# Kernel optimization log

Hardware: AMD Instinct MI355X
Metric: run time of the kernel (lower is better)

The kernel has to match this reference:

```python
import jax, jax.numpy as jnp
import numpy as np

DIM = 1024
HEADS = 16
DIM_HEAD = 64
INNER = HEADS * DIM_HEAD
SCALE = 8.0  # default scale in plain_cosine_sim_attention
EPS = 1e-5


def setup_inputs() -> dict:
    key = jax.random.key(0)
    ks = jax.random.split(key, 5)
    b, n = 2, 2048
    x = jax.random.normal(ks[0], (b, n, DIM), dtype=jnp.float32)
    ln_w = jnp.ones((DIM,), dtype=jnp.float32)
    ln_b = jnp.zeros((DIM,), dtype=jnp.float32)
    W_qkv = jax.random.normal(ks[1], (DIM, 3 * INNER), dtype=jnp.float32) * (DIM ** -0.5)
    W_out = jax.random.normal(ks[2], (INNER, DIM), dtype=jnp.float32) * (INNER ** -0.5)
    return {"x": x, "ln_w": ln_w, "ln_b": ln_b, "W_qkv": W_qkv, "W_out": W_out}


def _l2norm(t):
    return t / jnp.clip(jnp.linalg.norm(t, axis=-1, keepdims=True), 1e-12)


def reference(x, ln_w, ln_b, W_qkv, W_out):
    b, n, _ = x.shape
    # LayerNorm
    mu = jnp.mean(x, axis=-1, keepdims=True)
    var = jnp.var(x, axis=-1, keepdims=True)
    xn = (x - mu) * jax.lax.rsqrt(var + EPS) * ln_w + ln_b
    # QKV projection (no bias)
    qkv = xn @ W_qkv  # [b, n, 3*inner]
    q, k, v = jnp.split(qkv, 3, axis=-1)
    # [b, n, h*d] -> [b, h, n, d]
    def to_heads(t):
        return t.reshape(b, n, HEADS, DIM_HEAD).transpose(0, 2, 1, 3)
    q, k, v = to_heads(q), to_heads(k), to_heads(v)
    # cosine-sim attention: l2-normalize q, k then scaled dot product
    q = _l2norm(q)
    k = _l2norm(k)
    sim = jnp.einsum('bhid,bhjd->bhij', q, k) * SCALE
    # causal mask
    causal = jnp.tril(jnp.ones((n, n), dtype=bool))
    sim = jnp.where(causal, sim, jnp.finfo(sim.dtype).min)
    attn = jax.nn.softmax(sim, axis=-1)
    o = jnp.einsum('bhij,bhjd->bhid', attn, v)
    # [b, h, n, d] -> [b, n, h*d]
    o = o.transpose(0, 2, 1, 3).reshape(b, n, INNER)
    return o @ W_out
```

## Files before the change

### kernel.cpp

```cpp
#include <hip/hip_runtime.h>
#include <hip/hip_bf16.h>

typedef __attribute__((ext_vector_type(8))) short short8;
typedef __attribute__((ext_vector_type(4))) float floatx4;

__device__ __forceinline__ ushort f2bf(float f) {
    union { __hip_bfloat16 h; ushort u; } cv;
    cv.h = __float2bfloat16(f);
    return cv.u;
}
__device__ __forceinline__ float bf2f(ushort u) {
    union { ushort u; __hip_bfloat16 h; } cv;
    cv.u = u;
    return __bfloat162float(cv.h);
}
__device__ __forceinline__ ushort f2bf_rtz(float f) {
    union { float f; unsigned u; } cv;
    cv.f = f;
    return (ushort)(cv.u >> 16);
}

typedef __attribute__((address_space(1))) void* gas1_t;
typedef __attribute__((address_space(3))) void* las3_t;
__device__ __forceinline__ void cp16(const ushort* g, ushort* l) {
    __builtin_amdgcn_global_load_lds((gas1_t)(unsigned long long)g,
                                     (las3_t)(unsigned long long)l, 16, 0, 0);
}

__global__ __launch_bounds__(256) void prep_w_ln(const float* __restrict__ Wqkv,
                                                 const float* __restrict__ Wout,
                                                 ushort* __restrict__ WqkvT,
                                                 ushort* __restrict__ WoutT,
                                                 const float* __restrict__ x,
                                                 const float* __restrict__ lw,
                                                 const float* __restrict__ lb,
                                                 ushort* __restrict__ xn) {
    const int id = blockIdx.x;
    const int tid = threadIdx.x;
    if (id < 1024) {
        __shared__ float tile[64][65];
        const float* in; ushort* out; int C, bx, by;
        if (id < 768) { in = Wqkv; out = WqkvT; C = 3072; bx = id % 48; by = id / 48; }
        else { int i2 = id - 768; in = Wout; out = WoutT; C = 1024; bx = i2 & 15; by = i2 >> 4; }
        const int c0 = bx * 64, r0 = by * 64;
        const int tx = tid & 15, ty = tid >> 4;
        for (int j = 0; j < 4; j++) {
            int row = ty + j * 16;
            float4 v = *(const float4*)&in[(size_t)(r0 + row) * C + c0 + tx * 4];
            tile[tx * 4 + 0][row] = v.x;
            tile[tx * 4 + 1][row] = v.y;
            tile[tx * 4 + 2][row] = v.z;
            tile[tx * 4 + 3][row] = v.w;
        }
        __syncthreads();
        for (int j = 0; j < 4; j++) {
            int c_loc = ty + j * 16;
            ushort4 o;
            o.x = f2bf(tile[c_loc][tx * 4 + 0]);
            o.y = f2bf(tile[c_loc][tx * 4 + 1]);
            o.z = f2bf(tile[c_loc][tx * 4 + 2]);
            o.w = f2bf(tile[c_loc][tx * 4 + 3]);
            *(ushort4*)&out[(size_t)(c0 + c_loc) * 1024 + r0 + tx * 4] = o;
        }
    } else {
        int row = id - 1024;
        const float4* xr = (const float4*)(x + (size_t)row * 1024);
        float4 v = xr[tid];
        float s = v.x + v.y + v.z + v.w;
        float sq = v.x * v.x + v.y * v.y + v.z * v.z + v.w * v.w;
        for (int off = 32; off; off >>= 1) {
            s += __shfl_xor(s, off);
            sq += __shfl_xor(sq, off);
        }
        __shared__ float ls[4], lq[4];
        int wave = tid >> 6, lane = tid & 63;
        if (lane == 0) { ls[wave] = s; lq[wave] = sq; }
        __syncthreads();
        s = ls[0] + ls[1] + ls[2] + ls[3];
        sq = lq[0] + lq[1] + lq[2] + lq[3];
        float mu = s * (1.0f / 1024.0f);
        float var = sq * (1.0f / 1024.0f) - mu * mu;
        float rs = rsqrtf(var + 1e-5f);
        const float4* wr = (const float4*)lw;
        const float4* br = (const float4*)lb;
        float4 wv = wr[tid], bv = br[tid];
        ushort4 o;
        o.x = f2bf((v.x - mu) * rs * wv.x + bv.x);
        o.y = f2bf((v.y - mu) * rs * wv.y + bv.y);
        o.z = f2bf((v.z - mu) * rs * wv.z + bv.z);
        o.w = f2bf((v.w - mu) * rs * wv.w + bv.w);
        *(ushort4*)&xn[(size_t)row * 1024 + tid * 4] = o;
    }
}

__global__ __launch_bounds__(256) void gemm_qkv_fused(const ushort* __restrict__ A,
                                                      const ushort* __restrict__ Bt,
                                                      ushort* __restrict__ Qt,
                                                      ushort* __restrict__ Kt,
                                                      ushort* __restrict__ Vb) {
    __shared__ ushort smem[18432];
    const int K = 1024, T = 32;
    const int id = blockIdx.x;
    const int xcd = id & 7, r_ = id >> 3;
    const int bm = (xcd * 4 + r_ / 24) * 128;
    const int bn = r_ % 24;
    const int tid = threadIdx.x;
    const int wave = tid >> 6, lane = tid & 63;
    const int quad = lane >> 4, l15 = lane & 15;
    const int wm = (wave >> 1) * 64, wn = (wave & 1) * 64;

    const int s0 = tid, s1 = tid + 256;
    const int row0 = s0 >> 2, src0 = (s0 & 3) ^ (row0 & 3);
    const int row1 = s1 >> 2, src1 = (s1 & 3) ^ (row1 & 3);

    floatx4 acc[4][4];
    floatx4 z4 = {0.f, 0.f, 0.f, 0.f};
    for (int mi = 0; mi < 4; mi++)
        for (int ni = 0; ni < 4; ni++) acc[mi][ni] = z4;

    const ushort* Ap0 = A + (size_t)(bm + row0) * K + src0 * 8;
    const ushort* Ap1 = A + (size_t)(bm + row1) * K + src1 * 8;
    const ushort* Bp0 = Bt + (size_t)(bn * 128 + row0) * K + src0 * 8;
    const ushort* Bp1 = Bt + (size_t)(bn * 128 + row1) * K + src1 * 8;

    ushort* As = smem;
    ushort* Bs = smem + 8192;

    cp16(Ap0, &As[wave * 512]);
    cp16(Ap1, &As[2048 + wave * 512]);
    cp16(Bp0, &Bs[wave * 512]);
    cp16(Bp1, &Bs[2048 + wave * 512]);

    for (int t = 0; t < T; t++) {
        __syncthreads();
        if (t + 1 < T) {
            const int nb = (t + 1) & 1;
            const int k0n = (t + 1) << 5;
            cp16(Ap0 + k0n, &As[nb * 4096 + wave * 512]);
            cp16(Ap1 + k0n, &As[nb * 4096 + 2048 + wave * 512]);
            cp16(Bp0 + k0n, &Bs[nb * 4096 + wave * 512]);
            cp16(Bp1 + k0n, &Bs[nb * 4096 + 2048 + wave * 512]);
        }
        const ushort* Ab = As + (t & 1) * 4096;
        const ushort* Bb = Bs + (t & 1) * 4096;
        short8 af[4], bfr[4];
        for (int mi = 0; mi < 4; mi++) {
            int ra = wm + mi * 16 + l15;
            af[mi] = *(const short8*)&Ab[ra * 32 + ((quad ^ (ra & 3)) << 3)];
        }
        for (int ni = 0; ni < 4; ni++) {
            int rb = wn + ni * 16 + l15;
            bfr[ni] = *(const short8*)&Bb[rb * 32 + ((quad ^ (rb & 3)) << 3)];
        }
        for (int mi = 0; mi < 4; mi++)
            for (int ni = 0; ni < 4; ni++)
                acc[mi][ni] = __builtin_amdgcn_mfma_f32_16x16x32_bf16(
                    af[mi], bfr[ni], acc[mi][ni], 0, 0, 0);
    }

    const int col_base = bn * 128 + wn;
    const int type = col_base >> 10;
    const int h = (col_base & 1023) >> 6;
    const int row_base = bm + wm;

    if (type < 2) {
        ushort* dst = (type == 0) ? Qt : Kt;
        for (int mi = 0; mi < 4; mi++) {
            for (int r = 0; r < 4; r++) {
                float ss = 0.f;
                for (int ni = 0; ni < 4; ni++) ss += acc[mi][ni][r] * acc[mi][ni][r];
                for (int off = 1; off < 16; off <<= 1) ss += __shfl_xor(ss, off);
                float inv = rsqrtf(fmaxf(ss, 1e-24f));
                int rg = row_base + mi * 16 + quad * 4 + r;
                int bb = rg >> 11, n = rg & 2047;
                size_t orow = ((size_t)(bb * 16 + h) * 2048 + n) * 64;
                for (int ni = 0; ni < 4; ni++)
                    dst[orow + ni * 16 + l15] = f2bf(acc[mi][ni][r] * inv);
            }
        }
    } else {
        __syncthreads();
        ushort* tr = smem + wave * 4608;
        for (int mi = 0; mi < 4; mi++)
            for (int ni = 0; ni < 4; ni++)
                for (int r = 0; r < 4; r++) {
                    int row_l = mi * 16 + quad * 4 + r;
                    int col_l = ni * 16 + l15;
                    tr[col_l * 72 + row_l] = f2bf(acc[mi][ni][r]);
                }
        int bb = row_base >> 11, n0 = row_base & 2047;
        size_t vbase = ((size_t)(bb * 16 + h) * 32 + (n0 >> 6)) * 4096;
        const int dl = lane >> 3, nc = (lane & 7) * 8;
        for (int i = 0; i < 8; i++) {
            int d = dl + i * 8;
            short8 val = *(const short8*)&tr[d * 72 + nc];
            *(short8*)&Vb[vbase + (size_t)d * 64 + nc] = val;
        }
    }
}

__global__ __launch_bounds__(256) void gemm_out(const ushort* __restrict__ A,
                                                const ushort* __restrict__ Bt,
                                                float* __restrict__ C) {
    __shared__ ushort As[2][8192];
    __shared__ ushort Bs[2][4096];
    const int K = 1024, N = 1024;
    const int id = blockIdx.x;
    const int xcd = id & 7, r_ = id >> 3;
    const int bm = (xcd * 4 + (r_ >> 4)) * 128;
    const int bn = (r_ & 15) * 64;
    const int tid = threadIdx.x;
    const int wave = tid >> 6, lane = tid & 63;
    const int quad = lane >> 4, l15 = lane & 15;
    const int wm = (wave >> 1) * 64, wn = (wave & 1) * 32;

    const int ar0 = tid >> 3,          asg0 = (tid & 7) ^ (ar0 & 7);
    const int ar1 = (tid + 256) >> 3,  asg1 = (tid & 7) ^ (ar1 & 7);
    const int ar2 = (tid + 512) >> 3,  asg2 = (tid & 7) ^ (ar2 & 7);
    const int ar3 = (tid + 768) >> 3,  asg3 = (tid & 7) ^ (ar3 & 7);

    floatx4 acc[4][2];
    floatx4 z4 = {0.f, 0.f, 0.f, 0.f};
    for (int mi = 0; mi < 4; mi++)
        for (int ni = 0; ni < 2; ni++) acc[mi][ni] = z4;

    const ushort* Ap0 = A + (size_t)(bm + ar0) * K + asg0 * 8;
    const ushort* Ap1 = A + (size_t)(bm + ar1) * K + asg1 * 8;
    const ushort* Ap2 = A + (size_t)(bm + ar2) * K + asg2 * 8;
    const ushort* Ap3 = A + (size_t)(bm + ar3) * K + asg3 * 8;
    const ushort* Bp0 = Bt + (size_t)(bn + ar0) * K + asg0 * 8;
    const ushort* Bp1 = Bt + (size_t)(bn + ar1) * K + asg1 * 8;

    const int T = 16;
    cp16(Ap0, &As[0][wave * 512]);
    cp16(Ap1, &As[0][2048 + wave * 512]);
    cp16(Ap2, &As[0][4096 + wave * 512]);
    cp16(Ap3, &As[0][6144 + wave * 512]);
    cp16(Bp0, &Bs[0][wave * 512]);
    cp16(Bp1, &Bs[0][2048 + wave * 512]);

    for (int t = 0; t < T; t++) {
        __syncthreads();
        if (t + 1 < T) {
            const int nb = (t + 1) & 1;
            const int k0n = (t + 1) << 6;
            cp16(Ap0 + k0n, &As[nb][wave * 512]);
            cp16(Ap1 + k0n, &As[nb][2048 + wave * 512]);
            cp16(Ap2 + k0n, &As[nb][4096 + wave * 512]);
            cp16(Ap3 + k0n, &As[nb][6144 + wave * 512]);
            cp16(Bp0 + k0n, &Bs[nb][wave * 512]);
            cp16(Bp1 + k0n, &Bs[nb][2048 + wave * 512]);
        }
        const ushort* Ab = As[t & 1];
        const ushort* Bb = Bs[t & 1];
        short8 a0[4], a1[4], b0[2], b1[2];
        for (int mi = 0; mi < 4; mi++) {
            int ra = wm + mi * 16 + l15;
            a0[mi] = *(const short8*)&Ab[ra * 64 + ((quad ^ (ra & 7)) << 3)];
            a1[mi] = *(const short8*)&Ab[ra * 64 + (((quad + 4) ^ (ra & 7)) << 3)];
        }
        for (int ni = 0; ni < 2; ni++) {
            int rb = wn + ni * 16 + l15;
            b0[ni] = *(const short8*)&Bb[rb * 64 + ((quad ^ (rb & 7)) << 3)];
            b1[ni] = *(const short8*)&Bb[rb * 64 + (((quad + 4) ^ (rb & 7)) << 3)];
        }
        for (int mi = 0; mi < 4; mi++)
            for (int ni = 0; ni < 2; ni++) {
                acc[mi][ni] = __builtin_amdgcn_mfma_f32_16x16x32_bf16(
                    a0[mi], b0[ni], acc[mi][ni], 0, 0, 0);
                acc[mi][ni] = __builtin_amdgcn_mfma_f32_16x16x32_bf16(
                    a1[mi], b1[ni], acc[mi][ni], 0, 0, 0);
            }
    }
    for (int mi = 0; mi < 4; mi++)
        for (int ni = 0; ni < 2; ni++)
            for (int r = 0; r < 4; r++) {
                int row = bm + wm + mi * 16 + quad * 4 + r;
                int col = bn + wn + ni * 16 + l15;
                C[(size_t)row * N + col] = acc[mi][ni][r];
            }
}

#define LOG2E8 11.541560327111707f

__global__ __launch_bounds__(256) void flash_attn(const ushort* __restrict__ Qt,
                                                  const ushort* __restrict__ Kt,
                                                  const ushort* __restrict__ Vb,
                                                  ushort* __restrict__ O) {
    const int id = blockIdx.x;
    const int xcd = id & 7, r_ = id >> 3;
    const int bh = xcd + ((r_ & 3) << 3);
    const int u = r_ >> 2;
    const int s_ = u >> 3, g = u & 7;
    const int qt = (s_ == 0) ? g : (s_ == 1) ? (15 - g)
                 : (s_ == 2) ? (16 + g) : (31 - g);
    const int b = bh >> 4, h = bh & 15;
    const int tid = threadIdx.x;
    const int wave = tid >> 6, lane = tid & 63;
    const int quad = lane >> 4, l15 = lane & 15;

    __shared__ ushort Ks[2][64 * 64];
    __shared__ ushort Vs[2][64 * 64];
    __shared__ ushort Ps[4][16 * 64];

    const int ch0 = tid, ch1 = tid + 256;
    const int r0 = ch0 >> 3, sg0 = (ch0 & 7) ^ (r0 & 7);
    const int r1 = ch1 >> 3, sg1 = (ch1 & 7) ^ (r1 & 7);

    const ushort* Kp0 = Kt + ((size_t)bh * 2048 + r0) * 64 + sg0 * 8;
    const ushort* Kp1 = Kt + ((size_t)bh * 2048 + r1) * 64 + sg1 * 8;
    const ushort* Vp0 = Vb + (size_t)bh * 131072 + r0 * 64 + sg0 * 8;
    const ushort* Vp1 = Vb + (size_t)bh * 131072 + r1 * 64 + sg1 * 8;

    floatx4 z4 = {0.f, 0.f, 0.f, 0.f};

    const int q0 = qt * 64;
    const ushort* Qp = Qt + ((size_t)bh * 2048 + q0 + wave * 16 + l15) * 64;
    short8 qf0 = *(const short8*)(Qp + quad * 8);
    short8 qf1 = *(const short8*)(Qp + 32 + quad * 8);

    float rs_acc[4] = {0.f, 0.f, 0.f, 0.f};
    floatx4 o_acc[4];
    for (int ni = 0; ni < 4; ni++) o_acc[ni] = z4;

    cp16(Kp0, &Ks[0][wave * 512]);
    cp16(Kp1, &Ks[0][2048 + wave * 512]);
    short8 vA = *(const short8*)Vp0;
    short8 vB = *(const short8*)Vp1;
    *(short8*)&Vs[0][(unsigned)tid * 8] = vA;
    *(short8*)&Vs[0][(unsigned)(tid + 256) * 8] = vB;

    for (int kt = 0; kt <= qt; kt++) {
        __syncthreads();
        if (kt < qt) {
            const int nb2 = (kt + 1) & 1;
            const size_t to = (size_t)(kt + 1) * 4096;
            cp16(Kp0 + to, &Ks[nb2][wave * 512]);
            cp16(Kp1 + to, &Ks[nb2][2048 + wave * 512]);
            vA = *(const short8*)(Vp0 + to);
            vB = *(const short8*)(Vp1 + to);
        }
        const ushort* Kb = Ks[kt & 1];
        const ushort* Vbuf = Vs[kt & 1];

        floatx4 s_acc[4];
        for (int ni = 0; ni < 4; ni++) s_acc[ni] = z4;
        for (int ni = 0; ni < 4; ni++) {
            int rb = ni * 16 + l15;
            short8 kf0 = *(const short8*)&Kb[rb * 64 + ((quad ^ (rb & 7)) << 3)];
            short8 kf1 = *(const short8*)&Kb[rb * 64 + (((quad + 4) ^ (rb & 7)) << 3)];
            s_acc[ni] = __builtin_amdgcn_mfma_f32_16x16x32_bf16(qf0, kf0, s_acc[ni], 0, 0, 0);
            s_acc[ni] = __builtin_amdgcn_mfma_f32_16x16x32_bf16(qf1, kf1, s_acc[ni], 0, 0, 0);
        }

        const bool diag = (kt == qt);
        for (int ni = 0; ni < 4; ni++) {
            const int col_loc = ni * 16 + l15;
            const int chnk = col_loc >> 3;
            for (int r = 0; r < 4; r++) {
                const int row_l = quad * 4 + r;
                float e = __builtin_amdgcn_exp2f(
                    fmaf(s_acc[ni][r], LOG2E8, -LOG2E8));
                if (diag && col_loc > wave * 16 + row_l) e = 0.f;
                rs_acc[r] += e;
                Ps[wave][row_l * 64 + (((chnk ^ (row_l & 7)) << 3) | (col_loc & 7))] =
                    f2bf_rtz(e);
            }
        }

        short8 pa0 = *(const short8*)&Ps[wave][l15 * 64 + ((quad ^ (l15 & 7)) << 3)];
        short8 pa1 = *(const short8*)&Ps[wave][l15 * 64 + (((quad + 4) ^ (l15 & 7)) << 3)];
        for (int ni = 0; ni < 4; ni++) {
            int rv = ni * 16 + l15;
            short8 v0 = *(const short8*)&Vbuf[rv * 64 + ((quad ^ (rv & 7)) << 3)];
            short8 v1 = *(const short8*)&Vbuf[rv * 64 + (((quad + 4) ^ (rv & 7)) << 3)];
            o_acc[ni] = __builtin_amdgcn_mfma_f32_16x16x32_bf16(pa0, v0, o_acc[ni], 0, 0, 0);
            o_acc[ni] = __builtin_amdgcn_mfma_f32_16x16x32_bf16(pa1, v1, o_acc[ni], 0, 0, 0);
        }

        if (kt < qt) {
            ushort* Vn = Vs[(kt + 1) & 1];
            *(short8*)&Vn[(unsigned)tid * 8] = vA;
            *(short8*)&Vn[(unsigned)(tid + 256) * 8] = vB;
        }
    }

    for (int r = 0; r < 4; r++) {
        float rs = rs_acc[r];
        for (int off = 1; off < 16; off <<= 1) rs += __shfl_xor(rs, off);
        float inv = 1.0f / rs;
        int grow = q0 + wave * 16 + quad * 4 + r;
        size_t rowbase = ((size_t)b * 2048 + grow) * 1024 + h * 64;
        for (int ni = 0; ni < 4; ni++)
            O[rowbase + ni * 16 + l15] = f2bf(o_acc[ni][r] * inv);
    }
}

extern "C" void kernel_launch(void* const* d_in, const int* in_sizes, int n_in,
                              void* d_out, int out_size, void* d_ws, size_t ws_size,
                              hipStream_t stream) {
    const float* x = (const float*)d_in[0];
    const float* ln_w = (const float*)d_in[1];
    const float* ln_b = (const float*)d_in[2];
    const float* W_qkv = (const float*)d_in[3];
    const float* W_out = (const float*)d_in[4];

    char* w = (char*)d_ws;
    ushort* xn    = (ushort*)(w);
    ushort* obuf  = (ushort*)(w);
    ushort* WqkvT = (ushort*)(w + (8ull << 20));
    ushort* WoutT = (ushort*)(w + (14ull << 20));
    ushort* Vb    = (ushort*)(w + (16ull << 20));
    ushort* Qt    = (ushort*)(w + (24ull << 20));
    ushort* Kt    = (ushort*)(w + (32ull << 20));

    prep_w_ln<<<5120, 256, 0, stream>>>(W_qkv, W_out, WqkvT, WoutT, x, ln_w, ln_b, xn);
    gemm_qkv_fused<<<768, 256, 0, stream>>>(xn, WqkvT, Qt, Kt, Vb);
    flash_attn<<<1024, 256, 0, stream>>>(Qt, Kt, Vb, obuf);
    gemm_out<<<512, 256, 0, stream>>>(obuf, WoutT, (float*)d_out);
}
```

Baseline: 174.2 us.

## Use 128-row query tiles with 32x32x16 MFMA in flash attention

The attention kernel now handles 128 query rows per block, with each wave owning 32 rows, and switches from 16x16x32 to 32x32x16 bf16 MFMA. The grid is halved, and each K/V tile loaded into shared memory is reused by twice as many query rows, which cuts global and LDS traffic per flop. Waves whose rows end before the last key tile skip compute there but still take part in loads and barriers. The cost is more accumulator registers, a larger P buffer in LDS, fewer blocks in flight, and coarser causal load balance.

Result: slower. 185.2 us (+6.3%).

```diff
diff --git a/kernel.cpp b/kernel.cpp
--- a/kernel.cpp
+++ b/kernel.cpp
@@ -3,6 +3,7 @@
 
 typedef __attribute__((ext_vector_type(8))) short short8;
 typedef __attribute__((ext_vector_type(4))) float floatx4;
+typedef __attribute__((ext_vector_type(16))) float floatx16;
 
 __device__ __forceinline__ ushort f2bf(float f) {
     union { __hip_bfloat16 h; ushort u; } cv;
@@ -290,18 +291,16 @@
     const int id = blockIdx.x;
     const int xcd = id & 7, r_ = id >> 3;
     const int bh = xcd + ((r_ & 3) << 3);
-    const int u = r_ >> 2;
-    const int s_ = u >> 3, g = u & 7;
-    const int qt = (s_ == 0) ? g : (s_ == 1) ? (15 - g)
-                 : (s_ == 2) ? (16 + g) : (31 - g);
+    const int v_ = r_ >> 2;
+    const int t_ = (v_ < 8) ? v_ : 23 - v_;
     const int b = bh >> 4, h = bh & 15;
     const int tid = threadIdx.x;
     const int wave = tid >> 6, lane = tid & 63;
-    const int quad = lane >> 4, l15 = lane & 15;
+    const int c31 = lane & 31, hi = lane >> 5;
 
     __shared__ ushort Ks[2][64 * 64];
     __shared__ ushort Vs[2][64 * 64];
-    __shared__ ushort Ps[4][16 * 64];
+    __shared__ ushort Ps[4][32 * 64];
 
     const int ch0 = tid, ch1 = tid + 256;
     const int r0 = ch0 >> 3, sg0 = (ch0 & 7) ^ (r0 & 7);
@@ -312,16 +311,21 @@
     const ushort* Vp0 = Vb + (size_t)bh * 131072 + r0 * 64 + sg0 * 8;
     const ushort* Vp1 = Vb + (size_t)bh * 131072 + r1 * 64 + sg1 * 8;
 
-    floatx4 z4 = {0.f, 0.f, 0.f, 0.f};
-
-    const int q0 = qt * 64;
-    const ushort* Qp = Qt + ((size_t)bh * 2048 + q0 + wave * 16 + l15) * 64;
-    short8 qf0 = *(const short8*)(Qp + quad * 8);
-    short8 qf1 = *(const short8*)(Qp + 32 + quad * 8);
-
-    float rs_acc[4] = {0.f, 0.f, 0.f, 0.f};
-    floatx4 o_acc[4];
-    for (int ni = 0; ni < 4; ni++) o_acc[ni] = z4;
+    const int q0 = t_ * 128;
+    const int KT = 2 * t_ + 2;
+    const int lastkt = 2 * t_ + (wave >> 1);
+
+    const ushort* Qp = Qt + ((size_t)bh * 2048 + q0 + 32 * wave + c31) * 64;
+    short8 qa[4];
+#pragma unroll
+    for (int s = 0; s < 4; s++) qa[s] = *(const short8*)(Qp + s * 16 + hi * 8);
+
+    float rs_acc[16];
+#pragma unroll
+    for (int i = 0; i < 16; i++) rs_acc[i] = 0.f;
+    floatx16 oA[2];
+#pragma unroll
+    for (int i = 0; i < 16; i++) { oA[0][i] = 0.f; oA[1][i] = 0.f; }
 
     cp16(Kp0, &Ks[0][wave * 512]);
     cp16(Kp1, &Ks[0][2048 + wave * 512]);
@@ -330,9 +334,9 @@
     *(short8*)&Vs[0][(unsigned)tid * 8] = vA;
     *(short8*)&Vs[0][(unsigned)(tid + 256) * 8] = vB;
 
-    for (int kt = 0; kt <= qt; kt++) {
-        __syncthreads();
-        if (kt < qt) {
+    for (int kt = 0; kt < KT; kt++) {
+        __syncthreads();
+        if (kt + 1 < KT) {
             const int nb2 = (kt + 1) & 1;
             const size_t to = (size_t)(kt + 1) * 4096;
             cp16(Kp0 + to, &Ks[nb2][wave * 512]);
@@ -340,59 +344,81 @@
             vA = *(const short8*)(Vp0 + to);
             vB = *(const short8*)(Vp1 + to);
         }
-        const ushort* Kb = Ks[kt & 1];
-        const ushort* Vbuf = Vs[kt & 1];
-
-        floatx4 s_acc[4];
-        for (int ni = 0; ni < 4; ni++) s_acc[ni] = z4;
-        for (int ni = 0; ni < 4; ni++) {
-            int rb = ni * 16 + l15;
-            short8 kf0 = *(const short8*)&Kb[rb * 64 + ((quad ^ (rb & 7)) << 3)];
-            short8 kf1 = *(const short8*)&Kb[rb * 64 + (((quad + 4) ^ (rb & 7)) << 3)];
-            s_acc[ni] = __builtin_amdgcn_mfma_f32_16x16x32_bf16(qf0, kf0, s_acc[ni], 0, 0, 0);
-            s_acc[ni] = __builtin_amdgcn_mfma_f32_16x16x32_bf16(qf1, kf1, s_acc[ni], 0, 0, 0);
-        }
-
-        const bool diag = (kt == qt);
-        for (int ni = 0; ni < 4; ni++) {
-            const int col_loc = ni * 16 + l15;
-            const int chnk = col_loc >> 3;
-            for (int r = 0; r < 4; r++) {
-                const int row_l = quad * 4 + r;
-                float e = __builtin_amdgcn_exp2f(
-                    fmaf(s_acc[ni][r], LOG2E8, -LOG2E8));
-                if (diag && col_loc > wave * 16 + row_l) e = 0.f;
-                rs_acc[r] += e;
-                Ps[wave][row_l * 64 + (((chnk ^ (row_l & 7)) << 3) | (col_loc & 7))] =
-                    f2bf_rtz(e);
-            }
-        }
-
-        short8 pa0 = *(const short8*)&Ps[wave][l15 * 64 + ((quad ^ (l15 & 7)) << 3)];
-        short8 pa1 = *(const short8*)&Ps[wave][l15 * 64 + (((quad + 4) ^ (l15 & 7)) << 3)];
-        for (int ni = 0; ni < 4; ni++) {
-            int rv = ni * 16 + l15;
-            short8 v0 = *(const short8*)&Vbuf[rv * 64 + ((quad ^ (rv & 7)) << 3)];
-            short8 v1 = *(const short8*)&Vbuf[rv * 64 + (((quad + 4) ^ (rv & 7)) << 3)];
-            o_acc[ni] = __builtin_amdgcn_mfma_f32_16x16x32_bf16(pa0, v0, o_acc[ni], 0, 0, 0);
-            o_acc[ni] = __builtin_amdgcn_mfma_f32_16x16x32_bf16(pa1, v1, o_acc[ni], 0, 0, 0);
-        }
-
-        if (kt < qt) {
+
+        if (kt <= lastkt) {
+            const ushort* Kb = Ks[kt & 1];
+            const ushort* Vbuf = Vs[kt & 1];
+
+            floatx16 sA[2];
+#pragma unroll
+            for (int i = 0; i < 16; i++) { sA[0][i] = 0.f; sA[1][i] = 0.f; }
+#pragma unroll
+            for (int ni = 0; ni < 2; ni++) {
+                const int rb = 32 * ni + c31;
+#pragma unroll
+                for (int s = 0; s < 4; s++) {
+                    short8 kf = *(const short8*)&Kb[rb * 64 +
+                        (((2 * s + hi) ^ (rb & 7)) << 3)];
+                    sA[ni] = __builtin_amdgcn_mfma_f32_32x32x16_bf16(
+                        qa[s], kf, sA[ni], 0, 0, 0);
+                }
+            }
+
+            const bool diag = (kt == lastkt);
+            const int rowoff = (wave & 1) * 32;
+#pragma unroll
+            for (int ni = 0; ni < 2; ni++) {
+                const int c = 32 * ni + c31;
+                const int cc = c >> 3;
+#pragma unroll
+                for (int reg = 0; reg < 16; reg++) {
+                    const int rl = (reg & 3) + 8 * (reg >> 2) + 4 * hi;
+                    float e = __builtin_amdgcn_exp2f(
+                        fmaf(sA[ni][reg], LOG2E8, -LOG2E8));
+                    if (diag && c > rowoff + rl) e = 0.f;
+                    rs_acc[reg] += e;
+                    Ps[wave][rl * 64 + (((cc ^ (rl & 7)) << 3) | (c & 7))] =
+                        f2bf_rtz(e);
+                }
+            }
+
+            short8 pa[4];
+#pragma unroll
+            for (int s = 0; s < 4; s++)
+                pa[s] = *(const short8*)&Ps[wave][c31 * 64 +
+                    (((2 * s + hi) ^ (c31 & 7)) << 3)];
+
+#pragma unroll
+            for (int nj = 0; nj < 2; nj++) {
+                const int d = 32 * nj + c31;
+#pragma unroll
+                for (int s = 0; s < 4; s++) {
+                    short8 vf = *(const short8*)&Vbuf[d * 64 +
+                        (((2 * s + hi) ^ (d & 7)) << 3)];
+                    oA[nj] = __builtin_amdgcn_mfma_f32_32x32x16_bf16(
+                        pa[s], vf, oA[nj], 0, 0, 0);
+                }
+            }
+        }
+
+        if (kt + 1 < KT) {
             ushort* Vn = Vs[(kt + 1) & 1];
             *(short8*)&Vn[(unsigned)tid * 8] = vA;
             *(short8*)&Vn[(unsigned)(tid + 256) * 8] = vB;
         }
     }
 
-    for (int r = 0; r < 4; r++) {
-        float rs = rs_acc[r];
-        for (int off = 1; off < 16; off <<= 1) rs += __shfl_xor(rs, off);
-        float inv = 1.0f / rs;
-        int grow = q0 + wave * 16 + quad * 4 + r;
-        size_t rowbase = ((size_t)b * 2048 + grow) * 1024 + h * 64;
-        for (int ni = 0; ni < 4; ni++)
-            O[rowbase + ni * 16 + l15] = f2bf(o_acc[ni][r] * inv);
+#pragma unroll
+    for (int reg = 0; reg < 16; reg++) {
+        float rs = rs_acc[reg];
+        for (int off = 1; off < 32; off <<= 1) rs += __shfl_xor(rs, off);
+        const float inv = 1.0f / rs;
+        const int rl = (reg & 3) + 8 * (reg >> 2) + 4 * hi;
+        const int grow = q0 + 32 * wave + rl;
+        const size_t rowbase = ((size_t)b * 2048 + grow) * 1024 + h * 64;
+#pragma unroll
+        for (int nj = 0; nj < 2; nj++)
+            O[rowbase + 32 * nj + c31] = f2bf(oA[nj][reg] * inv);
     }
 }
 
@@ -416,6 +442,6 @@
 
     prep_w_ln<<<5120, 256, 0, stream>>>(W_qkv, W_out, WqkvT, WoutT, x, ln_w, ln_b, xn);
     gemm_qkv_fused<<<768, 256, 0, stream>>>(xn, WqkvT, Qt, Kt, Vb);
-    flash_attn<<<1024, 256, 0, stream>>>(Qt, Kt, Vb, obuf);
+    flash_attn<<<512, 256, 0, stream>>>(Qt, Kt, Vb, obuf);
     gemm_out<<<512, 256, 0, stream>>>(obuf, WoutT, (float*)d_out);
 }
```
